# Optimization experiments

Hardware: AMD Instinct MI355X
Metric: run time of the kernel (lower is better)

The kernel has to match this reference:

```python
import jax, jax.numpy as jnp
import numpy as np

TOP_K = 2

def setup_inputs() -> dict:
    key = jax.random.key(0)
    k1, k2, k3, k4, k5 = jax.random.split(key, 5)
    T, H, I, E = 2048, 2048, 2048, 8
    scale = 0.02
    return {
        "hidden_states": jax.random.normal(k1, (T, H), dtype=jnp.float32),
        "gate_w": jax.random.normal(k2, (E, H), dtype=jnp.float32) * scale,  # router Linear weight [E, H]
        "w1": jax.random.normal(k3, (E, H, I), dtype=jnp.float32) * scale,   # gate proj per expert
        "w3": jax.random.normal(k4, (E, H, I), dtype=jnp.float32) * scale,   # up proj per expert
        "w2": jax.random.normal(k5, (E, I, H), dtype=jnp.float32) * scale,   # down proj per expert
    }

def reference(hidden_states, gate_w, w1, w3, w2):
    T, H = hidden_states.shape
    E = gate_w.shape[0]
    # Router gate in float32 (ReplicatedLinear with params_dtype=float32, no bias)
    router_logits = jnp.einsum('th,eh->te', hidden_states.astype(jnp.float32), gate_w)
    probs = jax.nn.softmax(router_logits, axis=-1)  # [T, E]
    topk_w, topk_idx = jax.lax.top_k(probs, TOP_K)   # [T, K]
    topk_w = topk_w / jnp.sum(topk_w, axis=-1, keepdims=True)  # renormalize=True
    # Dense combine weights: zero for non-selected experts
    rows = jnp.arange(T)[:, None]
    comb = jnp.zeros((T, E), dtype=hidden_states.dtype).at[rows, topk_idx].add(
        topk_w.astype(hidden_states.dtype))
    # SwiGLU experts computed densely per expert, masked-combined
    g = jnp.einsum('th,ehi->tei', hidden_states, w1)   # gate proj
    u = jnp.einsum('th,ehi->tei', hidden_states, w3)   # up proj
    act = jax.nn.silu(g) * u                            # [T, E, I]
    y = jnp.einsum('tei,eih->teh', act, w2)             # down proj [T, E, H]
    out = jnp.einsum('te,teh->th', comb, y)             # weighted combine
    return out
```

## Files before the change

kernel.cpp:

```cpp
#include <hip/hip_runtime.h>
#include <hip/hip_bf16.h>

#define T_TOK 2048
#define H_DIM 2048
#define I_DIM 2048
#define E_NUM 8
#define TOPK  2

#define BM 128
#define BN 64
#define BK 64

typedef float  floatx4 __attribute__((ext_vector_type(4)));
typedef __bf16 bf16x8  __attribute__((ext_vector_type(8)));
typedef __bf16 bf16x4  __attribute__((ext_vector_type(4)));

__device__ __forceinline__ int swz(int row, int g) {
    return (row * 8 + (g ^ ((row >> 1) & 7))) * 16;
}

__global__ __launch_bounds__(64) void router_kernel(
    const float* __restrict__ hs, const float* __restrict__ gate_w,
    int* __restrict__ counts, int* __restrict__ lists, float* __restrict__ wpair,
    __bf16* __restrict__ Xbf)
{
    const int t    = blockIdx.x;
    const int lane = threadIdx.x;

    float acc[E_NUM];
#pragma unroll
    for (int e = 0; e < E_NUM; e++) acc[e] = 0.f;

    const float4* hsrow = (const float4*)(hs + (size_t)t * H_DIM);
#pragma unroll
    for (int it = 0; it < (H_DIM / 4) / 64; it++) {
        const int c = lane + it * 64;
        const float4 x = hsrow[c];
        const bf16x4 v = {(__bf16)x.x, (__bf16)x.y, (__bf16)x.z, (__bf16)x.w};
        *(bf16x4*)(Xbf + (size_t)t * H_DIM + 4 * c) = v;
#pragma unroll
        for (int e = 0; e < E_NUM; e++) {
            const float4 w = ((const float4*)(gate_w + (size_t)e * H_DIM))[c];
            acc[e] += x.x * w.x + x.y * w.y + x.z * w.z + x.w * w.w;
        }
    }
#pragma unroll
    for (int e = 0; e < E_NUM; e++) {
        float v = acc[e];
        for (int off = 32; off >= 1; off >>= 1) v += __shfl_xor(v, off, 64);
        acc[e] = v;
    }
    if (lane == 0) {
        float l0 = -1e30f; int i0 = 0;
        for (int e = 0; e < E_NUM; e++) if (acc[e] > l0) { l0 = acc[e]; i0 = e; }
        float l1 = -1e30f; int i1 = (i0 == 0) ? 1 : 0;
        for (int e = 0; e < E_NUM; e++) if (e != i0 && acc[e] > l1) { l1 = acc[e]; i1 = e; }
        const float e1 = __expf(l1 - l0);
        const float s  = 1.f + e1;
        const int p0 = atomicAdd(&counts[i0], 1);
        lists[i0 * T_TOK + p0] = 2 * t;
        const int p1 = atomicAdd(&counts[i1], 1);
        lists[i1 * T_TOK + p1] = 2 * t + 1;
        wpair[2 * t]     = 1.f / s;
        wpair[2 * t + 1] = e1 / s;
    }
}

__global__ __launch_bounds__(256, 3) void gemm1_kernel(
    const __bf16* __restrict__ Xbf, const float* __restrict__ w1,
    const float* __restrict__ w3, const int* __restrict__ counts,
    const int* __restrict__ lists, __bf16* __restrict__ Abuf)
{
    const int e   = blockIdx.z;
    const int n_e = counts[e];
    const int m0  = blockIdx.y * BM;
    if (m0 >= n_e) return;
    const int n0 = blockIdx.x * BN;

    const int*   list = lists + e * T_TOK;
    const float* w1e  = w1 + (size_t)e * H_DIM * I_DIM;
    const float* w3e  = w3 + (size_t)e * H_DIM * I_DIM;

    __shared__ __align__(16) __bf16 Xs [BM * BK];
    __shared__ __align__(16) __bf16 B1s[BN * BK];
    __shared__ __align__(16) __bf16 B3s[BN * BK];

    const int tid = threadIdx.x;
    const int xr8 = tid >> 3;
    const int xg  = tid & 7;
    const int kb = tid >> 5;
    const int np = tid & 31;

    int tok[4];
#pragma unroll
    for (int i = 0; i < 4; i++) {
        const int r = m0 + xr8 + 32 * i;
        tok[i] = (r < n_e) ? (list[r] >> 1) : 0;
    }

    const int wave = tid >> 6;
    const int lane = tid & 63;
    const int wm   = (wave >> 1) * 64;
    const int wn   = (wave & 1) * 32;
    const int lrow = lane & 15;
    const int quad = lane >> 4;

    floatx4 accG[4][2], accU[4][2];
#pragma unroll
    for (int i = 0; i < 4; i++)
#pragma unroll
        for (int j = 0; j < 2; j++) {
            accG[i][j] = (floatx4){0.f, 0.f, 0.f, 0.f};
            accU[i][j] = (floatx4){0.f, 0.f, 0.f, 0.f};
        }

    for (int k0 = 0; k0 < H_DIM; k0 += BK) {
#pragma unroll
        for (int i = 0; i < 4; i++) {
            const int m = xr8 + 32 * i;
            const bf16x8 v = *(const bf16x8*)(Xbf + (size_t)tok[i] * H_DIM + k0 + 8 * xg);
            *(bf16x8*)((char*)Xs + swz(m, xg)) = v;
        }
        {
            const float* src = w1e + (size_t)(k0 + 8 * kb) * I_DIM + n0 + 2 * np;
            float2 f[8];
#pragma unroll
            for (int j = 0; j < 8; j++) f[j] = *(const float2*)(src + (size_t)j * I_DIM);
            bf16x8 wlo, whi;
#pragma unroll
            for (int j = 0; j < 8; j++) { wlo[j] = (__bf16)f[j].x; whi[j] = (__bf16)f[j].y; }
            *(bf16x8*)((char*)B1s + swz(2 * np,     kb)) = wlo;
            *(bf16x8*)((char*)B1s + swz(2 * np + 1, kb)) = whi;
        }
        {
            const float* src = w3e + (size_t)(k0 + 8 * kb) * I_DIM + n0 + 2 * np;
            float2 f[8];
#pragma unroll
            for (int j = 0; j < 8; j++) f[j] = *(const float2*)(src + (size_t)j * I_DIM);
            bf16x8 wlo, whi;
#pragma unroll
            for (int j = 0; j < 8; j++) { wlo[j] = (__bf16)f[j].x; whi[j] = (__bf16)f[j].y; }
            *(bf16x8*)((char*)B3s + swz(2 * np,     kb)) = wlo;
            *(bf16x8*)((char*)B3s + swz(2 * np + 1, kb)) = whi;
        }
        __syncthreads();

#pragma unroll
        for (int s = 0; s < 2; s++) {
            bf16x8 af[4], b1f[2], b3f[2];
#pragma unroll
            for (int i = 0; i < 4; i++)
                af[i]  = *(const bf16x8*)((char*)Xs  + swz(wm + i * 16 + lrow, 4 * s + quad));
#pragma unroll
            for (int j = 0; j < 2; j++) {
                b1f[j] = *(const bf16x8*)((char*)B1s + swz(wn + j * 16 + lrow, 4 * s + quad));
                b3f[j] = *(const bf16x8*)((char*)B3s + swz(wn + j * 16 + lrow, 4 * s + quad));
            }
#pragma unroll
            for (int i = 0; i < 4; i++)
#pragma unroll
                for (int j = 0; j < 2; j++) {
                    accG[i][j] = __builtin_amdgcn_mfma_f32_16x16x32_bf16(af[i], b1f[j], accG[i][j], 0, 0, 0);
                    accU[i][j] = __builtin_amdgcn_mfma_f32_16x16x32_bf16(af[i], b3f[j], accU[i][j], 0, 0, 0);
                }
        }
        __syncthreads();
    }

#pragma unroll
    for (int i = 0; i < 4; i++) {
#pragma unroll
        for (int r = 0; r < 4; r++) {
            const int row = m0 + wm + i * 16 + quad * 4 + r;
            if (row < n_e) {
                const int p = list[row];
                __bf16* dst = Abuf + (size_t)p * I_DIM + n0 + wn + lrow;
#pragma unroll
                for (int j = 0; j < 2; j++) {
                    const float g = accG[i][j][r];
                    const float u = accU[i][j][r];
                    const float sv = g / (1.f + __expf(-g));
                    dst[j * 16] = (__bf16)(sv * u);
                }
            }
        }
    }
}

__global__ __launch_bounds__(256, 4) void gemm2_kernel(
    const __bf16* __restrict__ Abuf, const float* __restrict__ w2,
    const int* __restrict__ counts, const int* __restrict__ lists,
    __bf16* __restrict__ Ybuf)
{
    const int e   = blockIdx.z;
    const int n_e = counts[e];
    const int m0  = blockIdx.y * BM;
    if (m0 >= n_e) return;
    const int n0 = blockIdx.x * BN;

    const int*   list = lists + e * T_TOK;
    const float* w2e  = w2 + (size_t)e * I_DIM * H_DIM;

    __shared__ __align__(16) __bf16 As[BM * BK];
    __shared__ __align__(16) __bf16 Bs[BN * BK];

    const int tid = threadIdx.x;
    const int ar8 = tid >> 3;
    const int ag  = tid & 7;
    const int kb  = tid >> 5;
    const int np  = tid & 31;

    int prow[4];
#pragma unroll
    for (int i = 0; i < 4; i++) {
        const int r = m0 + ar8 + 32 * i;
        prow[i] = (r < n_e) ? list[r] : 0;
    }

    const int wave = tid >> 6;
    const int lane = tid & 63;
    const int wm   = (wave >> 1) * 64;
    const int wn   = (wave & 1) * 32;
    const int lrow = lane & 15;
    const int quad = lane >> 4;

    floatx4 acc[4][2];
#pragma unroll
    for (int i = 0; i < 4; i++)
#pragma unroll
        for (int j = 0; j < 2; j++) acc[i][j] = (floatx4){0.f, 0.f, 0.f, 0.f};

    for (int k0 = 0; k0 < I_DIM; k0 += BK) {
#pragma unroll
        for (int i = 0; i < 4; i++) {
            const int m = ar8 + 32 * i;
            const bf16x8 v = *(const bf16x8*)(Abuf + (size_t)prow[i] * I_DIM + k0 + 8 * ag);
            *(bf16x8*)((char*)As + swz(m, ag)) = v;
        }
        {
            const float* src = w2e + (size_t)(k0 + 8 * kb) * H_DIM + n0 + 2 * np;
            float2 f[8];
#pragma unroll
            for (int j = 0; j < 8; j++) f[j] = *(const float2*)(src + (size_t)j * H_DIM);
            bf16x8 wlo, whi;
#pragma unroll
            for (int j = 0; j < 8; j++) { wlo[j] = (__bf16)f[j].x; whi[j] = (__bf16)f[j].y; }
            *(bf16x8*)((char*)Bs + swz(2 * np,     kb)) = wlo;
            *(bf16x8*)((char*)Bs + swz(2 * np + 1, kb)) = whi;
        }
        __syncthreads();

#pragma unroll
        for (int s = 0; s < 2; s++) {
            bf16x8 af[4], bf[2];
#pragma unroll
            for (int i = 0; i < 4; i++)
                af[i] = *(const bf16x8*)((char*)As + swz(wm + i * 16 + lrow, 4 * s + quad));
#pragma unroll
            for (int j = 0; j < 2; j++)
                bf[j] = *(const bf16x8*)((char*)Bs + swz(wn + j * 16 + lrow, 4 * s + quad));
#pragma unroll
            for (int i = 0; i < 4; i++)
#pragma unroll
                for (int j = 0; j < 2; j++)
                    acc[i][j] = __builtin_amdgcn_mfma_f32_16x16x32_bf16(af[i], bf[j], acc[i][j], 0, 0, 0);
        }
        __syncthreads();
    }

#pragma unroll
    for (int i = 0; i < 4; i++) {
#pragma unroll
        for (int r = 0; r < 4; r++) {
            const int row = m0 + wm + i * 16 + quad * 4 + r;
            if (row < n_e) {
                const int p = list[row];
                __bf16* dst = Ybuf + (size_t)p * H_DIM + n0 + wn + lrow;
#pragma unroll
                for (int j = 0; j < 2; j++) dst[j * 16] = (__bf16)acc[i][j][r];
            }
        }
    }
}

__global__ __launch_bounds__(256) void combine_kernel(
    const __bf16* __restrict__ Ybuf, const float* __restrict__ wpair,
    float* __restrict__ out)
{
    const int idx = blockIdx.x * 256 + threadIdx.x;
    const int t   = idx >> 9;
    const int hc  = (idx & 511) * 4;
    const float w0 = wpair[2 * t];
    const float w1 = wpair[2 * t + 1];
    const __bf16* y0 = Ybuf + (size_t)(2 * t) * H_DIM + hc;
    const __bf16* y1 = y0 + H_DIM;
    float4 o;
    o.x = w0 * (float)y0[0] + w1 * (float)y1[0];
    o.y = w0 * (float)y0[1] + w1 * (float)y1[1];
    o.z = w0 * (float)y0[2] + w1 * (float)y1[2];
    o.w = w0 * (float)y0[3] + w1 * (float)y1[3];
    *(float4*)(out + (size_t)t * H_DIM + hc) = o;
}

extern "C" void kernel_launch(void* const* d_in, const int* in_sizes, int n_in,
                              void* d_out, int out_size, void* d_ws, size_t ws_size,
                              hipStream_t stream)
{
    const float* hs     = (const float*)d_in[0];
    const float* gate_w = (const float*)d_in[1];
    const float* w1     = (const float*)d_in[2];
    const float* w3     = (const float*)d_in[3];
    const float* w2     = (const float*)d_in[4];
    float*       out    = (float*)d_out;

    char* ws = (char*)d_ws;
    int*    counts = (int*)(ws + 0);
    float*  wpair  = (float*)(ws + 1024);
    int*    lists  = (int*)(ws + 32768);
    __bf16* Xbf    = (__bf16*)(ws + (1 << 17));
    __bf16* Ybuf   = (__bf16*)(ws + (1 << 17));
    __bf16* Abuf   = (__bf16*)(ws + (1 << 17) +
                               (size_t)2 * T_TOK * H_DIM * sizeof(__bf16));

    hipMemsetAsync(counts, 0, E_NUM * sizeof(int), stream);

    router_kernel<<<T_TOK, 64, 0, stream>>>(hs, gate_w, counts, lists, wpair, Xbf);

    gemm1_kernel<<<dim3(I_DIM / BN, T_TOK / BM, E_NUM), 256, 0, stream>>>(
        Xbf, w1, w3, counts, lists, Abuf);

    gemm2_kernel<<<dim3(H_DIM / BN, T_TOK / BM, E_NUM), 256, 0, stream>>>(
        Abuf, w2, counts, lists, Ybuf);

    combine_kernel<<<(T_TOK * H_DIM / 4) / 256, 256, 0, stream>>>(Ybuf, wpair, out);
}
```

Before: 598.0 us.

## Double-buffer LDS and prefetch two K-tiles ahead in both expert GEMMs

Both expert GEMM kernels now use ping-pong shared-memory buffers and register-staged global loads issued two tiles ahead. Global loads of weights and activations overlap MFMA compute, and each iteration needs one barrier instead of two. The cost is more registers and LDS per block, so the occupancy hints drop from 3 to 2 blocks for gemm1 and from 4 to 3 for gemm2.

Result: no change. 588.0 us (-1.7%).

```diff
diff --git a/kernel.cpp b/kernel.cpp
--- a/kernel.cpp
+++ b/kernel.cpp
@@ -10,6 +10,8 @@
 #define BM 128
 #define BN 64
 #define BK 64
+#define KT1 (H_DIM / BK)
+#define KT2 (I_DIM / BK)
 
 typedef float  floatx4 __attribute__((ext_vector_type(4)));
 typedef __bf16 bf16x8  __attribute__((ext_vector_type(8)));
@@ -18,6 +20,12 @@
 __device__ __forceinline__ int swz(int row, int g) {
     return (row * 8 + (g ^ ((row >> 1) & 7))) * 16;
 }
+
+#define PIPE_BARRIER() do { \
+    asm volatile("s_waitcnt lgkmcnt(0)" ::: "memory"); \
+    __builtin_amdgcn_s_barrier(); \
+    __builtin_amdgcn_sched_barrier(0); \
+} while (0)
 
 __global__ __launch_bounds__(64) void router_kernel(
     const float* __restrict__ hs, const float* __restrict__ gate_w,
@@ -66,7 +74,7 @@
     }
 }
 
-__global__ __launch_bounds__(256, 3) void gemm1_kernel(
+__global__ __launch_bounds__(256, 2) void gemm1_kernel(
     const __bf16* __restrict__ Xbf, const float* __restrict__ w1,
     const float* __restrict__ w3, const int* __restrict__ counts,
     const int* __restrict__ lists, __bf16* __restrict__ Abuf)
@@ -81,15 +89,15 @@
     const float* w1e  = w1 + (size_t)e * H_DIM * I_DIM;
     const float* w3e  = w3 + (size_t)e * H_DIM * I_DIM;
 
-    __shared__ __align__(16) __bf16 Xs [BM * BK];
-    __shared__ __align__(16) __bf16 B1s[BN * BK];
-    __shared__ __align__(16) __bf16 B3s[BN * BK];
+    __shared__ __align__(16) __bf16 Xs [2][BM * BK];
+    __shared__ __align__(16) __bf16 B1s[2][BN * BK];
+    __shared__ __align__(16) __bf16 B3s[2][BN * BK];
 
     const int tid = threadIdx.x;
     const int xr8 = tid >> 3;
     const int xg  = tid & 7;
-    const int kb = tid >> 5;
-    const int np = tid & 31;
+    const int kb  = tid >> 5;
+    const int np  = tid & 31;
 
     int tok[4];
 #pragma unroll
@@ -114,58 +122,89 @@
             accU[i][j] = (floatx4){0.f, 0.f, 0.f, 0.f};
         }
 
-    for (int k0 = 0; k0 < H_DIM; k0 += BK) {
-#pragma unroll
-        for (int i = 0; i < 4; i++) {
-            const int m = xr8 + 32 * i;
-            const bf16x8 v = *(const bf16x8*)(Xbf + (size_t)tok[i] * H_DIM + k0 + 8 * xg);
-            *(bf16x8*)((char*)Xs + swz(m, xg)) = v;
-        }
-        {
-            const float* src = w1e + (size_t)(k0 + 8 * kb) * I_DIM + n0 + 2 * np;
-            float2 f[8];
-#pragma unroll
-            for (int j = 0; j < 8; j++) f[j] = *(const float2*)(src + (size_t)j * I_DIM);
-            bf16x8 wlo, whi;
-#pragma unroll
-            for (int j = 0; j < 8; j++) { wlo[j] = (__bf16)f[j].x; whi[j] = (__bf16)f[j].y; }
-            *(bf16x8*)((char*)B1s + swz(2 * np,     kb)) = wlo;
-            *(bf16x8*)((char*)B1s + swz(2 * np + 1, kb)) = whi;
-        }
-        {
-            const float* src = w3e + (size_t)(k0 + 8 * kb) * I_DIM + n0 + 2 * np;
-            float2 f[8];
-#pragma unroll
-            for (int j = 0; j < 8; j++) f[j] = *(const float2*)(src + (size_t)j * I_DIM);
-            bf16x8 wlo, whi;
-#pragma unroll
-            for (int j = 0; j < 8; j++) { wlo[j] = (__bf16)f[j].x; whi[j] = (__bf16)f[j].y; }
-            *(bf16x8*)((char*)B3s + swz(2 * np,     kb)) = wlo;
-            *(bf16x8*)((char*)B3s + swz(2 * np + 1, kb)) = whi;
-        }
-        __syncthreads();
-
-#pragma unroll
-        for (int s = 0; s < 2; s++) {
-            bf16x8 af[4], b1f[2], b3f[2];
-#pragma unroll
-            for (int i = 0; i < 4; i++)
-                af[i]  = *(const bf16x8*)((char*)Xs  + swz(wm + i * 16 + lrow, 4 * s + quad));
-#pragma unroll
-            for (int j = 0; j < 2; j++) {
-                b1f[j] = *(const bf16x8*)((char*)B1s + swz(wn + j * 16 + lrow, 4 * s + quad));
-                b3f[j] = *(const bf16x8*)((char*)B3s + swz(wn + j * 16 + lrow, 4 * s + quad));
-            }
-#pragma unroll
-            for (int i = 0; i < 4; i++)
-#pragma unroll
-                for (int j = 0; j < 2; j++) {
-                    accG[i][j] = __builtin_amdgcn_mfma_f32_16x16x32_bf16(af[i], b1f[j], accG[i][j], 0, 0, 0);
-                    accU[i][j] = __builtin_amdgcn_mfma_f32_16x16x32_bf16(af[i], b3f[j], accU[i][j], 0, 0, 0);
-                }
-        }
-        __syncthreads();
-    }
+    bf16x8 xvA[4], xvB[4];
+    float2 f1A[8], f1B[8], f3A[8], f3B[8];
+
+#define G1_ISSUE(S, K0_) do { \
+    const __bf16* xp_ = Xbf + (K0_) + 8 * xg; \
+    _Pragma("unroll") \
+    for (int i = 0; i < 4; i++) { \
+        xv##S[i] = *(const bf16x8*)(xp_ + (size_t)tok[i] * H_DIM); \
+    } \
+    const float* s1_ = w1e + (size_t)((K0_) + 8 * kb) * I_DIM + n0 + 2 * np; \
+    const float* s3_ = w3e + (size_t)((K0_) + 8 * kb) * I_DIM + n0 + 2 * np; \
+    _Pragma("unroll") \
+    for (int j = 0; j < 8; j++) { \
+        f1##S[j] = *(const float2*)(s1_ + (size_t)j * I_DIM); \
+        f3##S[j] = *(const float2*)(s3_ + (size_t)j * I_DIM); \
+    } \
+    __builtin_amdgcn_sched_barrier(0); \
+} while (0)
+
+#define G1_WRITE(S, BUF) do { \
+    _Pragma("unroll") \
+    for (int i = 0; i < 4; i++) { \
+        *(bf16x8*)((char*)(Xs[BUF]) + swz(xr8 + 32 * i, xg)) = xv##S[i]; \
+    } \
+    bf16x8 wlo_, whi_; \
+    _Pragma("unroll") \
+    for (int j = 0; j < 8; j++) { wlo_[j] = (__bf16)f1##S[j].x; whi_[j] = (__bf16)f1##S[j].y; } \
+    *(bf16x8*)((char*)(B1s[BUF]) + swz(2 * np,     kb)) = wlo_; \
+    *(bf16x8*)((char*)(B1s[BUF]) + swz(2 * np + 1, kb)) = whi_; \
+    _Pragma("unroll") \
+    for (int j = 0; j < 8; j++) { wlo_[j] = (__bf16)f3##S[j].x; whi_[j] = (__bf16)f3##S[j].y; } \
+    *(bf16x8*)((char*)(B3s[BUF]) + swz(2 * np,     kb)) = wlo_; \
+    *(bf16x8*)((char*)(B3s[BUF]) + swz(2 * np + 1, kb)) = whi_; \
+} while (0)
+
+#define G1_COMPUTE(BUF) do { \
+    _Pragma("unroll") \
+    for (int s = 0; s < 2; s++) { \
+        bf16x8 af_[4], b1f_[2], b3f_[2]; \
+        _Pragma("unroll") \
+        for (int i = 0; i < 4; i++) { \
+            af_[i] = *(const bf16x8*)((char*)(Xs[BUF]) + swz(wm + i * 16 + lrow, 4 * s + quad)); \
+        } \
+        _Pragma("unroll") \
+        for (int j = 0; j < 2; j++) { \
+            b1f_[j] = *(const bf16x8*)((char*)(B1s[BUF]) + swz(wn + j * 16 + lrow, 4 * s + quad)); \
+            b3f_[j] = *(const bf16x8*)((char*)(B3s[BUF]) + swz(wn + j * 16 + lrow, 4 * s + quad)); \
+        } \
+        _Pragma("unroll") \
+        for (int i = 0; i < 4; i++) { \
+            _Pragma("unroll") \
+            for (int j = 0; j < 2; j++) { \
+                accG[i][j] = __builtin_amdgcn_mfma_f32_16x16x32_bf16(af_[i], b1f_[j], accG[i][j], 0, 0, 0); \
+                accU[i][j] = __builtin_amdgcn_mfma_f32_16x16x32_bf16(af_[i], b3f_[j], accU[i][j], 0, 0, 0); \
+            } \
+        } \
+    } \
+} while (0)
+
+    G1_ISSUE(A, 0);
+    G1_ISSUE(B, BK);
+    G1_WRITE(A, 0);
+    PIPE_BARRIER();
+
+#pragma unroll 1
+    for (int t = 1; t < KT1 - 1; t += 2) {
+        G1_ISSUE(A, (t + 1) * BK);
+        G1_COMPUTE(0);
+        G1_WRITE(B, 1);
+        PIPE_BARRIER();
+        G1_ISSUE(B, (t + 2) * BK);
+        G1_COMPUTE(1);
+        G1_WRITE(A, 0);
+        PIPE_BARRIER();
+    }
+    G1_COMPUTE(0);
+    G1_WRITE(B, 1);
+    PIPE_BARRIER();
+    G1_COMPUTE(1);
+
+#undef G1_ISSUE
+#undef G1_WRITE
+#undef G1_COMPUTE
 
 #pragma unroll
     for (int i = 0; i < 4; i++) {
@@ -187,7 +226,7 @@
     }
 }
 
-__global__ __launch_bounds__(256, 4) void gemm2_kernel(
+__global__ __launch_bounds__(256, 3) void gemm2_kernel(
     const __bf16* __restrict__ Abuf, const float* __restrict__ w2,
     const int* __restrict__ counts, const int* __restrict__ lists,
     __bf16* __restrict__ Ybuf)
@@ -201,8 +240,8 @@
     const int*   list = lists + e * T_TOK;
     const float* w2e  = w2 + (size_t)e * I_DIM * H_DIM;
 
-    __shared__ __align__(16) __bf16 As[BM * BK];
-    __shared__ __align__(16) __bf16 Bs[BN * BK];
+    __shared__ __align__(16) __bf16 As[2][BM * BK];
+    __shared__ __align__(16) __bf16 Bs[2][BN * BK];
 
     const int tid = threadIdx.x;
     const int ar8 = tid >> 3;
@@ -230,43 +269,81 @@
 #pragma unroll
         for (int j = 0; j < 2; j++) acc[i][j] = (floatx4){0.f, 0.f, 0.f, 0.f};
 
-    for (int k0 = 0; k0 < I_DIM; k0 += BK) {
-#pragma unroll
-        for (int i = 0; i < 4; i++) {
-            const int m = ar8 + 32 * i;
-            const bf16x8 v = *(const bf16x8*)(Abuf + (size_t)prow[i] * I_DIM + k0 + 8 * ag);
-            *(bf16x8*)((char*)As + swz(m, ag)) = v;
-        }
-        {
-            const float* src = w2e + (size_t)(k0 + 8 * kb) * H_DIM + n0 + 2 * np;
-            float2 f[8];
-#pragma unroll
-            for (int j = 0; j < 8; j++) f[j] = *(const float2*)(src + (size_t)j * H_DIM);
-            bf16x8 wlo, whi;
-#pragma unroll
-            for (int j = 0; j < 8; j++) { wlo[j] = (__bf16)f[j].x; whi[j] = (__bf16)f[j].y; }
-            *(bf16x8*)((char*)Bs + swz(2 * np,     kb)) = wlo;
-            *(bf16x8*)((char*)Bs + swz(2 * np + 1, kb)) = whi;
-        }
-        __syncthreads();
-
-#pragma unroll
-        for (int s = 0; s < 2; s++) {
-            bf16x8 af[4], bf[2];
-#pragma unroll
-            for (int i = 0; i < 4; i++)
-                af[i] = *(const bf16x8*)((char*)As + swz(wm + i * 16 + lrow, 4 * s + quad));
-#pragma unroll
-            for (int j = 0; j < 2; j++)
-                bf[j] = *(const bf16x8*)((char*)Bs + swz(wn + j * 16 + lrow, 4 * s + quad));
-#pragma unroll
-            for (int i = 0; i < 4; i++)
-#pragma unroll
-                for (int j = 0; j < 2; j++)
-                    acc[i][j] = __builtin_amdgcn_mfma_f32_16x16x32_bf16(af[i], bf[j], acc[i][j], 0, 0, 0);
-        }
-        __syncthreads();
-    }
+    bf16x8 avA[4], avB[4];
+    float2 f2A[8], f2B[8];
+
+#define G2_ISSUE(S, K0_) do { \
+    const __bf16* ap_ = Abuf + (K0_) + 8 * ag; \
+    _Pragma("unroll") \
+    for (int i = 0; i < 4; i++) { \
+        av##S[i] = *(const bf16x8*)(ap_ + (size_t)prow[i] * I_DIM); \
+    } \
+    const float* s2_ = w2e + (size_t)((K0_) + 8 * kb) * H_DIM + n0 + 2 * np; \
+    _Pragma("unroll") \
+    for (int j = 0; j < 8; j++) { \
+        f2##S[j] = *(const float2*)(s2_ + (size_t)j * H_DIM); \
+    } \
+    __builtin_amdgcn_sched_barrier(0); \
+} while (0)
+
+#define G2_WRITE(S, BUF) do { \
+    _Pragma("unroll") \
+    for (int i = 0; i < 4; i++) { \
+        *(bf16x8*)((char*)(As[BUF]) + swz(ar8 + 32 * i, ag)) = av##S[i]; \
+    } \
+    bf16x8 wlo_, whi_; \
+    _Pragma("unroll") \
+    for (int j = 0; j < 8; j++) { wlo_[j] = (__bf16)f2##S[j].x; whi_[j] = (__bf16)f2##S[j].y; } \
+    *(bf16x8*)((char*)(Bs[BUF]) + swz(2 * np,     kb)) = wlo_; \
+    *(bf16x8*)((char*)(Bs[BUF]) + swz(2 * np + 1, kb)) = whi_; \
+} while (0)
+
+#define G2_COMPUTE(BUF) do { \
+    _Pragma("unroll") \
+    for (int s = 0; s < 2; s++) { \
+        bf16x8 af_[4], bf_[2]; \
+        _Pragma("unroll") \
+        for (int i = 0; i < 4; i++) { \
+            af_[i] = *(const bf16x8*)((char*)(As[BUF]) + swz(wm + i * 16 + lrow, 4 * s + quad)); \
+        } \
+        _Pragma("unroll") \
+        for (int j = 0; j < 2; j++) { \
+            bf_[j] = *(const bf16x8*)((char*)(Bs[BUF]) + swz(wn + j * 16 + lrow, 4 * s + quad)); \
+        } \
+        _Pragma("unroll") \
+        for (int i = 0; i < 4; i++) { \
+            _Pragma("unroll") \
+            for (int j = 0; j < 2; j++) { \
+                acc[i][j] = __builtin_amdgcn_mfma_f32_16x16x32_bf16(af_[i], bf_[j], acc[i][j], 0, 0, 0); \
+            } \
+        } \
+    } \
+} while (0)
+
+    G2_ISSUE(A, 0);
+    G2_ISSUE(B, BK);
+    G2_WRITE(A, 0);
+    PIPE_BARRIER();
+
+#pragma unroll 1
+    for (int t = 1; t < KT2 - 1; t += 2) {
+        G2_ISSUE(A, (t + 1) * BK);
+        G2_COMPUTE(0);
+        G2_WRITE(B, 1);
+        PIPE_BARRIER();
+        G2_ISSUE(B, (t + 2) * BK);
+        G2_COMPUTE(1);
+        G2_WRITE(A, 0);
+        PIPE_BARRIER();
+    }
+    G2_COMPUTE(0);
+    G2_WRITE(B, 1);
+    PIPE_BARRIER();
+    G2_COMPUTE(1);
+
+#undef G2_ISSUE
+#undef G2_WRITE
+#undef G2_COMPUTE
 
 #pragma unroll
     for (int i = 0; i < 4; i++) {
```

## Use direct global-to-LDS loads for activations and widen weight loads and gemm2 tile

Applied to the files above, without the earlier changes.

Activation tiles in both GEMMs are now loaded with global_load_lds, straight into shared memory, with the swizzle folded into the source address. This removes the register round-trip. Weight tiles are read as float4 per thread, with the w1/w3 loads split across the two thread halves, which lowers per-thread load count. gemm2 moves to a 128-wide N tile with more accumulators and fewer blocks, launch bound lowered to 3. The combine kernel uses vector bf16 loads. The cost is higher register pressure in gemm2, and the swizzle mapping must match the layout the MFMA reads expect.

Result: no change. 592.9 us (-0.8%).

```diff
diff --git a/kernel.cpp b/kernel.cpp
--- a/kernel.cpp
+++ b/kernel.cpp
@@ -5,11 +5,11 @@
 #define H_DIM 2048
 #define I_DIM 2048
 #define E_NUM 8
-#define TOPK  2
-
-#define BM 128
-#define BN 64
-#define BK 64
+
+#define BM  128
+#define BK  64
+#define BN1 64
+#define BN2 128
 
 typedef float  floatx4 __attribute__((ext_vector_type(4)));
 typedef __bf16 bf16x8  __attribute__((ext_vector_type(8)));
@@ -17,6 +17,12 @@
 
 __device__ __forceinline__ int swz(int row, int g) {
     return (row * 8 + (g ^ ((row >> 1) & 7))) * 16;
+}
+
+typedef const __attribute__((address_space(1))) void* as1_cptr;
+typedef __attribute__((address_space(3))) void*       as3_ptr;
+__device__ __forceinline__ void glds16(const void* g, void* l) {
+    __builtin_amdgcn_global_load_lds((as1_cptr)g, (as3_ptr)l, 16, 0, 0);
 }
 
 __global__ __launch_bounds__(64) void router_kernel(
@@ -75,31 +81,36 @@
     const int n_e = counts[e];
     const int m0  = blockIdx.y * BM;
     if (m0 >= n_e) return;
-    const int n0 = blockIdx.x * BN;
-
-    const int*   list = lists + e * T_TOK;
-    const float* w1e  = w1 + (size_t)e * H_DIM * I_DIM;
-    const float* w3e  = w3 + (size_t)e * H_DIM * I_DIM;
+    const int n0 = blockIdx.x * BN1;
+
+    const int* list = lists + e * T_TOK;
 
     __shared__ __align__(16) __bf16 Xs [BM * BK];
-    __shared__ __align__(16) __bf16 B1s[BN * BK];
-    __shared__ __align__(16) __bf16 B3s[BN * BK];
-
-    const int tid = threadIdx.x;
-    const int xr8 = tid >> 3;
-    const int xg  = tid & 7;
-    const int kb = tid >> 5;
-    const int np = tid & 31;
-
-    int tok[4];
-#pragma unroll
-    for (int i = 0; i < 4; i++) {
-        const int r = m0 + xr8 + 32 * i;
-        tok[i] = (r < n_e) ? (list[r] >> 1) : 0;
-    }
-
+    __shared__ __align__(16) __bf16 B1s[BN1 * BK];
+    __shared__ __align__(16) __bf16 B3s[BN1 * BK];
+
+    const int tid  = threadIdx.x;
     const int wave = tid >> 6;
     const int lane = tid & 63;
+
+    size_t xoff[4];
+#pragma unroll
+    for (int i = 0; i < 4; i++) {
+        const int row = wave * 32 + i * 8 + (lane >> 3);
+        const int r   = m0 + row;
+        const int tok = (r < n_e) ? (list[r] >> 1) : 0;
+        const int g   = (lane & 7) ^ ((4 * i + (lane >> 4)) & 7);
+        xoff[i] = (size_t)tok * H_DIM + 8 * g;
+    }
+
+    const int half = tid >> 7;
+    const int t7   = tid & 127;
+    const int wnp  = t7 & 15;
+    const int wkb  = t7 >> 4;
+    const float* wsrc = (half ? w3 : w1) + (size_t)e * H_DIM * I_DIM
+                      + (size_t)(8 * wkb) * I_DIM + n0 + 4 * wnp;
+    __bf16* wdst = half ? B3s : B1s;
+
     const int wm   = (wave >> 1) * 64;
     const int wn   = (wave & 1) * 32;
     const int lrow = lane & 15;
@@ -116,32 +127,20 @@
 
     for (int k0 = 0; k0 < H_DIM; k0 += BK) {
 #pragma unroll
-        for (int i = 0; i < 4; i++) {
-            const int m = xr8 + 32 * i;
-            const bf16x8 v = *(const bf16x8*)(Xbf + (size_t)tok[i] * H_DIM + k0 + 8 * xg);
-            *(bf16x8*)((char*)Xs + swz(m, xg)) = v;
-        }
+        for (int i = 0; i < 4; i++)
+            glds16(Xbf + xoff[i] + k0, Xs + (wave * 4 + i) * 512);
         {
-            const float* src = w1e + (size_t)(k0 + 8 * kb) * I_DIM + n0 + 2 * np;
-            float2 f[8];
-#pragma unroll
-            for (int j = 0; j < 8; j++) f[j] = *(const float2*)(src + (size_t)j * I_DIM);
-            bf16x8 wlo, whi;
-#pragma unroll
-            for (int j = 0; j < 8; j++) { wlo[j] = (__bf16)f[j].x; whi[j] = (__bf16)f[j].y; }
-            *(bf16x8*)((char*)B1s + swz(2 * np,     kb)) = wlo;
-            *(bf16x8*)((char*)B1s + swz(2 * np + 1, kb)) = whi;
-        }
-        {
-            const float* src = w3e + (size_t)(k0 + 8 * kb) * I_DIM + n0 + 2 * np;
-            float2 f[8];
-#pragma unroll
-            for (int j = 0; j < 8; j++) f[j] = *(const float2*)(src + (size_t)j * I_DIM);
-            bf16x8 wlo, whi;
-#pragma unroll
-            for (int j = 0; j < 8; j++) { wlo[j] = (__bf16)f[j].x; whi[j] = (__bf16)f[j].y; }
-            *(bf16x8*)((char*)B3s + swz(2 * np,     kb)) = wlo;
-            *(bf16x8*)((char*)B3s + swz(2 * np + 1, kb)) = whi;
+            const float* s = wsrc + (size_t)k0 * I_DIM;
+            floatx4 f[8];
+#pragma unroll
+            for (int j = 0; j < 8; j++) f[j] = *(const floatx4*)(s + (size_t)j * I_DIM);
+#pragma unroll
+            for (int c = 0; c < 4; c++) {
+                bf16x8 gcol;
+#pragma unroll
+                for (int j = 0; j < 8; j++) gcol[j] = (__bf16)f[j][c];
+                *(bf16x8*)((char*)wdst + swz(4 * wnp + c, wkb)) = gcol;
+            }
         }
         __syncthreads();
 
@@ -187,7 +186,7 @@
     }
 }
 
-__global__ __launch_bounds__(256, 4) void gemm2_kernel(
+__global__ __launch_bounds__(256, 3) void gemm2_kernel(
     const __bf16* __restrict__ Abuf, const float* __restrict__ w2,
     const int* __restrict__ counts, const int* __restrict__ lists,
     __bf16* __restrict__ Ybuf)
@@ -196,73 +195,75 @@
     const int n_e = counts[e];
     const int m0  = blockIdx.y * BM;
     if (m0 >= n_e) return;
-    const int n0 = blockIdx.x * BN;
+    const int n0 = blockIdx.x * BN2;
 
     const int*   list = lists + e * T_TOK;
     const float* w2e  = w2 + (size_t)e * I_DIM * H_DIM;
 
     __shared__ __align__(16) __bf16 As[BM * BK];
-    __shared__ __align__(16) __bf16 Bs[BN * BK];
-
-    const int tid = threadIdx.x;
-    const int ar8 = tid >> 3;
-    const int ag  = tid & 7;
-    const int kb  = tid >> 5;
-    const int np  = tid & 31;
-
-    int prow[4];
-#pragma unroll
-    for (int i = 0; i < 4; i++) {
-        const int r = m0 + ar8 + 32 * i;
-        prow[i] = (r < n_e) ? list[r] : 0;
-    }
-
+    __shared__ __align__(16) __bf16 Bs[BN2 * BK];
+
+    const int tid  = threadIdx.x;
     const int wave = tid >> 6;
     const int lane = tid & 63;
+
+    size_t aoff[4];
+#pragma unroll
+    for (int i = 0; i < 4; i++) {
+        const int row = wave * 32 + i * 8 + (lane >> 3);
+        const int r   = m0 + row;
+        const int p   = (r < n_e) ? list[r] : 0;
+        const int g   = (lane & 7) ^ ((4 * i + (lane >> 4)) & 7);
+        aoff[i] = (size_t)p * I_DIM + 8 * g;
+    }
+
+    const int np = tid & 31;
+    const int kb = tid >> 5;
+    const float* wsrc = w2e + (size_t)(8 * kb) * H_DIM + n0 + 4 * np;
+
     const int wm   = (wave >> 1) * 64;
-    const int wn   = (wave & 1) * 32;
+    const int wn   = (wave & 1) * 64;
     const int lrow = lane & 15;
     const int quad = lane >> 4;
 
-    floatx4 acc[4][2];
+    floatx4 acc[4][4];
 #pragma unroll
     for (int i = 0; i < 4; i++)
 #pragma unroll
-        for (int j = 0; j < 2; j++) acc[i][j] = (floatx4){0.f, 0.f, 0.f, 0.f};
+        for (int j = 0; j < 4; j++) acc[i][j] = (floatx4){0.f, 0.f, 0.f, 0.f};
 
     for (int k0 = 0; k0 < I_DIM; k0 += BK) {
 #pragma unroll
-        for (int i = 0; i < 4; i++) {
-            const int m = ar8 + 32 * i;
-            const bf16x8 v = *(const bf16x8*)(Abuf + (size_t)prow[i] * I_DIM + k0 + 8 * ag);
-            *(bf16x8*)((char*)As + swz(m, ag)) = v;
-        }
+        for (int i = 0; i < 4; i++)
+            glds16(Abuf + aoff[i] + k0, As + (wave * 4 + i) * 512);
         {
-            const float* src = w2e + (size_t)(k0 + 8 * kb) * H_DIM + n0 + 2 * np;
-            float2 f[8];
-#pragma unroll
-            for (int j = 0; j < 8; j++) f[j] = *(const float2*)(src + (size_t)j * H_DIM);
-            bf16x8 wlo, whi;
-#pragma unroll
-            for (int j = 0; j < 8; j++) { wlo[j] = (__bf16)f[j].x; whi[j] = (__bf16)f[j].y; }
-            *(bf16x8*)((char*)Bs + swz(2 * np,     kb)) = wlo;
-            *(bf16x8*)((char*)Bs + swz(2 * np + 1, kb)) = whi;
+            const float* s = wsrc + (size_t)k0 * H_DIM;
+            floatx4 f[8];
+#pragma unroll
+            for (int j = 0; j < 8; j++) f[j] = *(const floatx4*)(s + (size_t)j * H_DIM);
+#pragma unroll
+            for (int c = 0; c < 4; c++) {
+                bf16x8 gcol;
+#pragma unroll
+                for (int j = 0; j < 8; j++) gcol[j] = (__bf16)f[j][c];
+                *(bf16x8*)((char*)Bs + swz(4 * np + c, kb)) = gcol;
+            }
         }
         __syncthreads();
 
 #pragma unroll
         for (int s = 0; s < 2; s++) {
-            bf16x8 af[4], bf[2];
+            bf16x8 af[4], bf[4];
 #pragma unroll
             for (int i = 0; i < 4; i++)
                 af[i] = *(const bf16x8*)((char*)As + swz(wm + i * 16 + lrow, 4 * s + quad));
 #pragma unroll
-            for (int j = 0; j < 2; j++)
+            for (int j = 0; j < 4; j++)
                 bf[j] = *(const bf16x8*)((char*)Bs + swz(wn + j * 16 + lrow, 4 * s + quad));
 #pragma unroll
             for (int i = 0; i < 4; i++)
 #pragma unroll
-                for (int j = 0; j < 2; j++)
+                for (int j = 0; j < 4; j++)
                     acc[i][j] = __builtin_amdgcn_mfma_f32_16x16x32_bf16(af[i], bf[j], acc[i][j], 0, 0, 0);
         }
         __syncthreads();
@@ -277,7 +278,7 @@
                 const int p = list[row];
                 __bf16* dst = Ybuf + (size_t)p * H_DIM + n0 + wn + lrow;
 #pragma unroll
-                for (int j = 0; j < 2; j++) dst[j * 16] = (__bf16)acc[i][j][r];
+                for (int j = 0; j < 4; j++) dst[j * 16] = (__bf16)acc[i][j][r];
             }
         }
     }
@@ -294,11 +295,13 @@
     const float w1 = wpair[2 * t + 1];
     const __bf16* y0 = Ybuf + (size_t)(2 * t) * H_DIM + hc;
     const __bf16* y1 = y0 + H_DIM;
+    const bf16x4 a0 = *(const bf16x4*)y0;
+    const bf16x4 a1 = *(const bf16x4*)y1;
     float4 o;
-    o.x = w0 * (float)y0[0] + w1 * (float)y1[0];
-    o.y = w0 * (float)y0[1] + w1 * (float)y1[1];
-    o.z = w0 * (float)y0[2] + w1 * (float)y1[2];
-    o.w = w0 * (float)y0[3] + w1 * (float)y1[3];
+    o.x = w0 * (float)a0[0] + w1 * (float)a1[0];
+    o.y = w0 * (float)a0[1] + w1 * (float)a1[1];
+    o.z = w0 * (float)a0[2] + w1 * (float)a1[2];
+    o.w = w0 * (float)a0[3] + w1 * (float)a1[3];
     *(float4*)(out + (size_t)t * H_DIM + hc) = o;
 }
 
@@ -326,10 +329,10 @@
 
     router_kernel<<<T_TOK, 64, 0, stream>>>(hs, gate_w, counts, lists, wpair, Xbf);
 
-    gemm1_kernel<<<dim3(I_DIM / BN, T_TOK / BM, E_NUM), 256, 0, stream>>>(
+    gemm1_kernel<<<dim3(I_DIM / BN1, T_TOK / BM, E_NUM), 256, 0, stream>>>(
         Xbf, w1, w3, counts, lists, Abuf);
 
-    gemm2_kernel<<<dim3(H_DIM / BN, T_TOK / BM, E_NUM), 256, 0, stream>>>(
+    gemm2_kernel<<<dim3(H_DIM / BN2, T_TOK / BM, E_NUM), 256, 0, stream>>>(
         Abuf, w2, counts, lists, Ybuf);
 
     combine_kernel<<<(T_TOK * H_DIM / 4) / 256, 256, 0, stream>>>(Ybuf, wpair, out);
```

## Halve GEMM row tile, load activations via global_load_lds, vectorize combine loads

Applied to the files above, without the earlier changes.

Shrinks the M tile of both expert GEMMs from 128 to 64 rows and raises the occupancy hint to 6 blocks per CU. The gathered activation rows now go straight from global memory into LDS through the global_load_lds builtin, with the swizzle applied on the source address instead of staging through registers. The combine kernel reads bf16x4 vectors instead of scalars. The smaller tile gives more blocks and less padding waste per expert, but each block now reuses every fp32 weight tile for only 64 rows, so total weight traffic and conversion work double.

New measurement: 705.8 us. +18.0%, slower.

```diff
diff --git a/kernel.cpp b/kernel.cpp
--- a/kernel.cpp
+++ b/kernel.cpp
@@ -5,9 +5,8 @@
 #define H_DIM 2048
 #define I_DIM 2048
 #define E_NUM 8
-#define TOPK  2
-
-#define BM 128
+
+#define BM 64
 #define BN 64
 #define BK 64
 
@@ -17,6 +16,12 @@
 
 __device__ __forceinline__ int swz(int row, int g) {
     return (row * 8 + (g ^ ((row >> 1) & 7))) * 16;
+}
+
+typedef const __attribute__((address_space(1))) void* as1_cptr;
+typedef __attribute__((address_space(3))) void*       as3_ptr;
+__device__ __forceinline__ void glds16(const void* g, void* l) {
+    __builtin_amdgcn_global_load_lds((as1_cptr)g, (as3_ptr)l, 16, 0, 0);
 }
 
 __global__ __launch_bounds__(64) void router_kernel(
@@ -66,7 +71,7 @@
     }
 }
 
-__global__ __launch_bounds__(256, 3) void gemm1_kernel(
+__global__ __launch_bounds__(256, 6) void gemm1_kernel(
     const __bf16* __restrict__ Xbf, const float* __restrict__ w1,
     const float* __restrict__ w3, const int* __restrict__ counts,
     const int* __restrict__ lists, __bf16* __restrict__ Abuf)
@@ -85,29 +90,33 @@
     __shared__ __align__(16) __bf16 B1s[BN * BK];
     __shared__ __align__(16) __bf16 B3s[BN * BK];
 
-    const int tid = threadIdx.x;
-    const int xr8 = tid >> 3;
-    const int xg  = tid & 7;
-    const int kb = tid >> 5;
-    const int np = tid & 31;
-
-    int tok[4];
-#pragma unroll
-    for (int i = 0; i < 4; i++) {
-        const int r = m0 + xr8 + 32 * i;
-        tok[i] = (r < n_e) ? (list[r] >> 1) : 0;
-    }
-
+    const int tid  = threadIdx.x;
     const int wave = tid >> 6;
     const int lane = tid & 63;
-    const int wm   = (wave >> 1) * 64;
+
+    size_t xoff[2];
+#pragma unroll
+    for (int i = 0; i < 2; i++) {
+        const int row = wave * 16 + i * 8 + (lane >> 3);
+        const int r   = m0 + row;
+        const int tok = (r < n_e) ? (list[r] >> 1) : 0;
+        const int g   = (lane & 7) ^ ((4 * i + (lane >> 4)) & 7);
+        xoff[i] = (size_t)tok * H_DIM + 8 * g;
+    }
+
+    const int np = tid & 31;
+    const int kb = tid >> 5;
+    const float* s1 = w1e + (size_t)(8 * kb) * I_DIM + n0 + 2 * np;
+    const float* s3 = w3e + (size_t)(8 * kb) * I_DIM + n0 + 2 * np;
+
+    const int wm   = (wave >> 1) * 32;
     const int wn   = (wave & 1) * 32;
     const int lrow = lane & 15;
     const int quad = lane >> 4;
 
-    floatx4 accG[4][2], accU[4][2];
-#pragma unroll
-    for (int i = 0; i < 4; i++)
+    floatx4 accG[2][2], accU[2][2];
+#pragma unroll
+    for (int i = 0; i < 2; i++)
 #pragma unroll
         for (int j = 0; j < 2; j++) {
             accG[i][j] = (floatx4){0.f, 0.f, 0.f, 0.f};
@@ -116,16 +125,13 @@
 
     for (int k0 = 0; k0 < H_DIM; k0 += BK) {
 #pragma unroll
-        for (int i = 0; i < 4; i++) {
-            const int m = xr8 + 32 * i;
-            const bf16x8 v = *(const bf16x8*)(Xbf + (size_t)tok[i] * H_DIM + k0 + 8 * xg);
-            *(bf16x8*)((char*)Xs + swz(m, xg)) = v;
-        }
+        for (int i = 0; i < 2; i++)
+            glds16(Xbf + xoff[i] + k0, Xs + (wave * 2 + i) * 512);
         {
-            const float* src = w1e + (size_t)(k0 + 8 * kb) * I_DIM + n0 + 2 * np;
+            const float* s = s1 + (size_t)k0 * I_DIM;
             float2 f[8];
 #pragma unroll
-            for (int j = 0; j < 8; j++) f[j] = *(const float2*)(src + (size_t)j * I_DIM);
+            for (int j = 0; j < 8; j++) f[j] = *(const float2*)(s + (size_t)j * I_DIM);
             bf16x8 wlo, whi;
 #pragma unroll
             for (int j = 0; j < 8; j++) { wlo[j] = (__bf16)f[j].x; whi[j] = (__bf16)f[j].y; }
@@ -133,10 +139,10 @@
             *(bf16x8*)((char*)B1s + swz(2 * np + 1, kb)) = whi;
         }
         {
-            const float* src = w3e + (size_t)(k0 + 8 * kb) * I_DIM + n0 + 2 * np;
+            const float* s = s3 + (size_t)k0 * I_DIM;
             float2 f[8];
 #pragma unroll
-            for (int j = 0; j < 8; j++) f[j] = *(const float2*)(src + (size_t)j * I_DIM);
+            for (int j = 0; j < 8; j++) f[j] = *(const float2*)(s + (size_t)j * I_DIM);
             bf16x8 wlo, whi;
 #pragma unroll
             for (int j = 0; j < 8; j++) { wlo[j] = (__bf16)f[j].x; whi[j] = (__bf16)f[j].y; }
@@ -147,9 +153,9 @@
 
 #pragma unroll
         for (int s = 0; s < 2; s++) {
-            bf16x8 af[4], b1f[2], b3f[2];
-#pragma unroll
-            for (int i = 0; i < 4; i++)
+            bf16x8 af[2], b1f[2], b3f[2];
+#pragma unroll
+            for (int i = 0; i < 2; i++)
                 af[i]  = *(const bf16x8*)((char*)Xs  + swz(wm + i * 16 + lrow, 4 * s + quad));
 #pragma unroll
             for (int j = 0; j < 2; j++) {
@@ -157,7 +163,7 @@
                 b3f[j] = *(const bf16x8*)((char*)B3s + swz(wn + j * 16 + lrow, 4 * s + quad));
             }
 #pragma unroll
-            for (int i = 0; i < 4; i++)
+            for (int i = 0; i < 2; i++)
 #pragma unroll
                 for (int j = 0; j < 2; j++) {
                     accG[i][j] = __builtin_amdgcn_mfma_f32_16x16x32_bf16(af[i], b1f[j], accG[i][j], 0, 0, 0);
@@ -168,7 +174,7 @@
     }
 
 #pragma unroll
-    for (int i = 0; i < 4; i++) {
+    for (int i = 0; i < 2; i++) {
 #pragma unroll
         for (int r = 0; r < 4; r++) {
             const int row = m0 + wm + i * 16 + quad * 4 + r;
@@ -187,7 +193,7 @@
     }
 }
 
-__global__ __launch_bounds__(256, 4) void gemm2_kernel(
+__global__ __launch_bounds__(256, 6) void gemm2_kernel(
     const __bf16* __restrict__ Abuf, const float* __restrict__ w2,
     const int* __restrict__ counts, const int* __restrict__ lists,
     __bf16* __restrict__ Ybuf)
@@ -204,44 +210,44 @@
     __shared__ __align__(16) __bf16 As[BM * BK];
     __shared__ __align__(16) __bf16 Bs[BN * BK];
 
-    const int tid = threadIdx.x;
-    const int ar8 = tid >> 3;
-    const int ag  = tid & 7;
-    const int kb  = tid >> 5;
-    const int np  = tid & 31;
-
-    int prow[4];
-#pragma unroll
-    for (int i = 0; i < 4; i++) {
-        const int r = m0 + ar8 + 32 * i;
-        prow[i] = (r < n_e) ? list[r] : 0;
-    }
-
+    const int tid  = threadIdx.x;
     const int wave = tid >> 6;
     const int lane = tid & 63;
-    const int wm   = (wave >> 1) * 64;
+
+    size_t aoff[2];
+#pragma unroll
+    for (int i = 0; i < 2; i++) {
+        const int row = wave * 16 + i * 8 + (lane >> 3);
+        const int r   = m0 + row;
+        const int p   = (r < n_e) ? list[r] : 0;
+        const int g   = (lane & 7) ^ ((4 * i + (lane >> 4)) & 7);
+        aoff[i] = (size_t)p * I_DIM + 8 * g;
+    }
+
+    const int np = tid & 31;
+    const int kb = tid >> 5;
+    const float* s2 = w2e + (size_t)(8 * kb) * H_DIM + n0 + 2 * np;
+
+    const int wm   = (wave >> 1) * 32;
     const int wn   = (wave & 1) * 32;
     const int lrow = lane & 15;
     const int quad = lane >> 4;
 
-    floatx4 acc[4][2];
-#pragma unroll
-    for (int i = 0; i < 4; i++)
+    floatx4 acc[2][2];
+#pragma unroll
+    for (int i = 0; i < 2; i++)
 #pragma unroll
         for (int j = 0; j < 2; j++) acc[i][j] = (floatx4){0.f, 0.f, 0.f, 0.f};
 
     for (int k0 = 0; k0 < I_DIM; k0 += BK) {
 #pragma unroll
-        for (int i = 0; i < 4; i++) {
-            const int m = ar8 + 32 * i;
-            const bf16x8 v = *(const bf16x8*)(Abuf + (size_t)prow[i] * I_DIM + k0 + 8 * ag);
-            *(bf16x8*)((char*)As + swz(m, ag)) = v;
-        }
+        for (int i = 0; i < 2; i++)
+            glds16(Abuf + aoff[i] + k0, As + (wave * 2 + i) * 512);
         {
-            const float* src = w2e + (size_t)(k0 + 8 * kb) * H_DIM + n0 + 2 * np;
+            const float* s = s2 + (size_t)k0 * H_DIM;
             float2 f[8];
 #pragma unroll
-            for (int j = 0; j < 8; j++) f[j] = *(const float2*)(src + (size_t)j * H_DIM);
+            for (int j = 0; j < 8; j++) f[j] = *(const float2*)(s + (size_t)j * H_DIM);
             bf16x8 wlo, whi;
 #pragma unroll
             for (int j = 0; j < 8; j++) { wlo[j] = (__bf16)f[j].x; whi[j] = (__bf16)f[j].y; }
@@ -252,15 +258,15 @@
 
 #pragma unroll
         for (int s = 0; s < 2; s++) {
-            bf16x8 af[4], bf[2];
-#pragma unroll
-            for (int i = 0; i < 4; i++)
+            bf16x8 af[2], bf[2];
+#pragma unroll
+            for (int i = 0; i < 2; i++)
                 af[i] = *(const bf16x8*)((char*)As + swz(wm + i * 16 + lrow, 4 * s + quad));
 #pragma unroll
             for (int j = 0; j < 2; j++)
                 bf[j] = *(const bf16x8*)((char*)Bs + swz(wn + j * 16 + lrow, 4 * s + quad));
 #pragma unroll
-            for (int i = 0; i < 4; i++)
+            for (int i = 0; i < 2; i++)
 #pragma unroll
                 for (int j = 0; j < 2; j++)
                     acc[i][j] = __builtin_amdgcn_mfma_f32_16x16x32_bf16(af[i], bf[j], acc[i][j], 0, 0, 0);
@@ -269,7 +275,7 @@
     }
 
 #pragma unroll
-    for (int i = 0; i < 4; i++) {
+    for (int i = 0; i < 2; i++) {
 #pragma unroll
         for (int r = 0; r < 4; r++) {
             const int row = m0 + wm + i * 16 + quad * 4 + r;
@@ -294,11 +300,13 @@
     const float w1 = wpair[2 * t + 1];
     const __bf16* y0 = Ybuf + (size_t)(2 * t) * H_DIM + hc;
     const __bf16* y1 = y0 + H_DIM;
+    const bf16x4 a0 = *(const bf16x4*)y0;
+    const bf16x4 a1 = *(const bf16x4*)y1;
     float4 o;
-    o.x = w0 * (float)y0[0] + w1 * (float)y1[0];
-    o.y = w0 * (float)y0[1] + w1 * (float)y1[1];
-    o.z = w0 * (float)y0[2] + w1 * (float)y1[2];
-    o.w = w0 * (float)y0[3] + w1 * (float)y1[3];
+    o.x = w0 * (float)a0[0] + w1 * (float)a1[0];
+    o.y = w0 * (float)a0[1] + w1 * (float)a1[1];
+    o.z = w0 * (float)a0[2] + w1 * (float)a1[2];
+    o.w = w0 * (float)a0[3] + w1 * (float)a1[3];
     *(float4*)(out + (size_t)t * H_DIM + hc) = o;
 }
 
```
